# Optimization experiments

Hardware: AMD Instinct MI355X
Metric: run time of the kernel (lower is better)

## Reference

```python
import jax, jax.numpy as jnp
import numpy as np

B, T, V, D, U = 256, 1024, 6, 64, 64  # batch, seq, vocab, embed dim, lstm units


def _lstm_dir(x_seq, mask_seq, Wk, Wr, b, reverse):
    # x_seq: [B,T,D], mask_seq: [B,T] bool. Keras gate order: i, f, g(cell), o.
    Bc, Tc, _ = x_seq.shape
    Uc = Wr.shape[0]
    if reverse:
        x_seq = x_seq[:, ::-1, :]
        mask_seq = mask_seq[:, ::-1]
    # precompute input projections for all timesteps (one big GEMM)
    xproj = jnp.einsum('btd,dg->tbg', x_seq, Wk) + b          # [T,B,4U]
    m = jnp.swapaxes(mask_seq, 0, 1)[..., None]               # [T,B,1]

    def step(carry, inp):
        h, c = carry
        xp, mt = inp
        z = xp + h @ Wr                                        # [B,4U]
        i, f, g, o = jnp.split(z, 4, axis=-1)
        i = jax.nn.sigmoid(i)
        f = jax.nn.sigmoid(f)
        g = jnp.tanh(g)
        o = jax.nn.sigmoid(o)
        c_new = f * c + i * g
        h_new = o * jnp.tanh(c_new)
        # masked steps carry state through and repeat previous output
        h = jnp.where(mt, h_new, h)
        c = jnp.where(mt, c_new, c)
        return (h, c), h

    h0 = jnp.zeros((Bc, Uc), x_seq.dtype)
    _, ys = jax.lax.scan(step, (h0, h0), (xproj, m))           # ys: [T,B,U]
    ys = jnp.swapaxes(ys, 0, 1)                                # [B,T,U]
    if reverse:
        ys = ys[:, ::-1, :]
    return ys


def reference(tokens, emb, Wk_f, Wr_f, b_f, Wk_b, Wr_b, b_b, Wd, bd):
    x = emb[tokens]                                            # [B,T,D]
    mask = jnp.any(x != 0, axis=-1)                            # Masking(0): all-zero feature vec -> masked
    y_f = _lstm_dir(x, mask, Wk_f, Wr_f, b_f, reverse=False)   # [B,T,U]
    y_b = _lstm_dir(x, mask, Wk_b, Wr_b, b_b, reverse=True)    # [B,T,U]
    y = jnp.concatenate([y_f, y_b], axis=-1)                   # [B,T,2U]
    last = y[:, -1, :]                                         # [B,2U]
    return last @ Wd + bd                                      # [B,1]


def setup_inputs() -> dict:
    key = jax.random.key(0)
    ks = jax.random.split(key, 8)
    return {
        'tokens': jax.random.randint(ks[0], (B, T), 0, V, dtype=jnp.int32),
        'emb': jax.random.normal(ks[1], (V, D), dtype=jnp.float32),
        'Wk_f': jax.random.normal(ks[2], (D, 4 * U), dtype=jnp.float32) * 0.05,
        'Wr_f': jax.random.normal(ks[3], (U, 4 * U), dtype=jnp.float32) * 0.05,
        'b_f': jnp.zeros((4 * U,), dtype=jnp.float32),
        'Wk_b': jax.random.normal(ks[4], (D, 4 * U), dtype=jnp.float32) * 0.05,
        'Wr_b': jax.random.normal(ks[5], (U, 4 * U), dtype=jnp.float32) * 0.05,
        'b_b': jnp.zeros((4 * U,), dtype=jnp.float32),
        'Wd': jax.random.normal(ks[6], (2 * U, 1), dtype=jnp.float32) * 0.05,
        'bd': jnp.zeros((1,), dtype=jnp.float32),
    }
```

## Files before the change

### kernel.cpp

```cpp
#include <hip/hip_runtime.h>


constexpr int kB = 256;
constexpr int kT = 1024;
constexpr int kV = 6;
constexpr int kD = 64;
constexpr int kU = 64;
constexpr int kG = 256;

#define LOG2E 1.44269504f

typedef _Float16 v2h __attribute__((ext_vector_type(2)));

template <int CTRL>
__device__ __forceinline__ float dppf(float x) {
    return __int_as_float(
        __builtin_amdgcn_mov_dpp(__float_as_int(x), CTRL, 0xF, 0xF, true));
}
constexpr int kXor1 = 0xB1;
constexpr int kXor2 = 0x4E;
constexpr int kBc0 = 0x00, kBc1 = 0x55, kBc2 = 0xAA, kBc3 = 0xFF;

__device__ __forceinline__ float fast_rcp(float x) { return __builtin_amdgcn_rcpf(x); }
__device__ __forceinline__ float exp2_f(float x)   { return __builtin_amdgcn_exp2f(x); }
__device__ __forceinline__ float sig_f(float z)  { return fast_rcp(1.0f + exp2_f(-LOG2E * z)); }
__device__ __forceinline__ float tanh_f(float z) { return 2.0f * fast_rcp(1.0f + exp2_f(-2.0f * LOG2E * z)) - 1.0f; }

__device__ __forceinline__ v2h as_v2h(float x) { return __builtin_bit_cast(v2h, x); }

__global__ __launch_bounds__(256, 1) void bilstm_last_kernel(
    const int*   __restrict__ tokens,
    const float* __restrict__ emb,
    const float* __restrict__ Wk_f,
    const float* __restrict__ Wr_f,
    const float* __restrict__ b_f,
    const float* __restrict__ Wk_b,
    const float* __restrict__ b_b,
    const float* __restrict__ Wd,
    const float* __restrict__ bd,
    float*       __restrict__ out)
{
    __shared__ float s_emb[kV * kD];
    __shared__ float s_projP[kV * kG];
    __shared__ int   s_tok[kT];
    __shared__ _Float16 __align__(16) s_hh[2][kU];
    __shared__ float s_act[kG];

    const int b   = blockIdx.x;
    const int tid = threadIdx.x;
    const int l   = tid & 63;
    const int wv  = tid >> 6;
    const int s   = l & 3;
    const int k   = l >> 2;
    const int u   = wv * 16 + k;

    for (int i = tid; i < kV * kD; i += 256) s_emb[i] = emb[i];
    ((int4*)s_tok)[tid] = ((const int4*)(tokens + b * kT))[tid];
    if (tid < kU) { s_hh[0][tid] = (_Float16)0.f; s_hh[1][tid] = (_Float16)0.f; }
    __syncthreads();

    unsigned int mbv = 0;
#pragma unroll
    for (int v = 0; v < kV; ++v) {
        const unsigned long long bb = __ballot(s_emb[v * kD + l] != 0.0f);
        mbv |= (bb != 0ull) ? (1u << v) : 0u;
    }
    const unsigned int smb = __builtin_amdgcn_readfirstlane(mbv);

    const int tokL = s_tok[kT - 1];

    float a0 = b_f[tid], a1 = a0, a2 = a0, a3 = a0, a4 = a0, a5 = a0;
    float accb = b_b[tid];
    for (int d = 0; d < kD; ++d) {
        const float wkf = Wk_f[d * kG + tid];
        const float wkb = Wk_b[d * kG + tid];
        a0 = fmaf(s_emb[0 * kD + d], wkf, a0);
        a1 = fmaf(s_emb[1 * kD + d], wkf, a1);
        a2 = fmaf(s_emb[2 * kD + d], wkf, a2);
        a3 = fmaf(s_emb[3 * kD + d], wkf, a3);
        a4 = fmaf(s_emb[4 * kD + d], wkf, a4);
        a5 = fmaf(s_emb[5 * kD + d], wkf, a5);
        accb = fmaf(s_emb[tokL * kD + d], wkb, accb);
    }
    {
        const int g0 = tid >> 6, u0 = tid & 63, w0 = u0 >> 4, k0 = u0 & 15;
        const int q = w0 * 64 + k0 * 4 + g0;
        s_projP[0 * kG + q] = a0;
        s_projP[1 * kG + q] = a1;
        s_projP[2 * kG + q] = a2;
        s_projP[3 * kG + q] = a3;
        s_projP[4 * kG + q] = a4;
        s_projP[5 * kG + q] = a5;
    }

    float ab;
    if (tid < 128)      ab = sig_f(accb);
    else if (tid < 192) ab = tanh_f(accb);
    else                ab = sig_f(accb);
    s_act[tid] = ab;
    __syncthreads();
    float hb_val = 0.0f;
    if (tid < kU) {
        const float cb = s_act[tid] * s_act[2 * kU + tid];
        const float hb = s_act[3 * kU + tid] * tanh_f(cb);
        hb_val = ((smb >> tokL) & 1) ? hb : 0.0f;
    }

#define DECLH(g, p)                                                         \
    v2h wh##g##_##p;                                                        \
    wh##g##_##p.x = (_Float16)Wr_f[(16 * s + 2 * p + 0) * kG + (g * 64 + u)]; \
    wh##g##_##p.y = (_Float16)Wr_f[(16 * s + 2 * p + 1) * kG + (g * 64 + u)];
    DECLH(0,0) DECLH(0,1) DECLH(0,2) DECLH(0,3) DECLH(0,4) DECLH(0,5) DECLH(0,6) DECLH(0,7)
    DECLH(1,0) DECLH(1,1) DECLH(1,2) DECLH(1,3) DECLH(1,4) DECLH(1,5) DECLH(1,6) DECLH(1,7)
    DECLH(2,0) DECLH(2,1) DECLH(2,2) DECLH(2,3) DECLH(2,4) DECLH(2,5) DECLH(2,6) DECLH(2,7)
    DECLH(3,0) DECLH(3,1) DECLH(3,2) DECLH(3,3) DECLH(3,4) DECLH(3,5) DECLH(3,6) DECLH(3,7)
#undef DECLH

    const bool  isg    = (s == 2);
    const float aScale = isg ? -2.0f * LOG2E : -LOG2E;
    const float aMul   = isg ? 2.0f : 1.0f;
    const float aAdd   = isg ? -1.0f : 0.0f;

    float c = 0.0f, hreg = 0.0f;
    __syncthreads();

    int stok0 = __builtin_amdgcn_readfirstlane(s_tok[0]);
    float zcur = s_projP[stok0 * kG + tid];
    int   mskc = (smb >> stok0) & 1;
    int   stokA = __builtin_amdgcn_readfirstlane(s_tok[1]);

#define DOTG(g)                                                               \
        float pa##g = __builtin_amdgcn_fdot2(H0, wh##g##_0, 0.0f, false);     \
        float pb##g = __builtin_amdgcn_fdot2(H1, wh##g##_1, 0.0f, false);     \
        pa##g = __builtin_amdgcn_fdot2(H2, wh##g##_2, pa##g, false);          \
        pb##g = __builtin_amdgcn_fdot2(H3, wh##g##_3, pb##g, false);          \
        pa##g = __builtin_amdgcn_fdot2(H4, wh##g##_4, pa##g, false);          \
        pb##g = __builtin_amdgcn_fdot2(H5, wh##g##_5, pb##g, false);          \
        pa##g = __builtin_amdgcn_fdot2(H6, wh##g##_6, pa##g, false);          \
        pb##g = __builtin_amdgcn_fdot2(H7, wh##g##_7, pb##g, false);          \
        float p##g = pa##g + pb##g;

#define STEP(RP, WP, TT)                                                      \
    {                                                                         \
                        \
        const float4* hp = (const float4*)s_hh[RP];                           \
        const float4 hv0 = hp[s * 2 + 0];                                     \
        const float4 hv1 = hp[s * 2 + 1];                                     \
                    \
        const int   vtokB = s_tok[((TT) + 2) & (kT - 1)];                     \
        const float znext = s_projP[stokA * kG + tid];                        \
        const int   mskn  = (int)((smb >> stokA) & 1);                        \
        const v2h H0 = as_v2h(hv0.x), H1 = as_v2h(hv0.y);                     \
        const v2h H2 = as_v2h(hv0.z), H3 = as_v2h(hv0.w);                     \
        const v2h H4 = as_v2h(hv1.x), H5 = as_v2h(hv1.y);                     \
        const v2h H6 = as_v2h(hv1.z), H7 = as_v2h(hv1.w);                     \
        DOTG(0) DOTG(1) DOTG(2) DOTG(3)                                       \
                         \
        p0 += dppf<kXor1>(p0); p1 += dppf<kXor1>(p1);                         \
        p2 += dppf<kXor1>(p2); p3 += dppf<kXor1>(p3);                         \
        \
        float X = (s & 1) ? p1 : p0;                                          \
        float Y = (s & 1) ? p3 : p2;                                          \
        X += dppf<kXor2>(X); Y += dppf<kXor2>(Y);                             \
        const float z = ((s & 2) ? Y : X) + zcur;                             \
                                      \
        const float e = exp2_f(z * aScale);                                   \
        const float r = fast_rcp(1.0f + e);                                   \
        const float a = fmaf(r, aMul, aAdd);                                  \
                     \
        const float ai = dppf<kBc0>(a);                                       \
        const float af = dppf<kBc1>(a);                                       \
        const float ag = dppf<kBc2>(a);                                       \
        const float ao = dppf<kBc3>(a);                                       \
        const float cn = fmaf(af, c, ai * ag);                                \
        const float hn = ao * tanh_f(cn);                                     \
        if (mskc) { c = cn; hreg = hn; }                  \
        if (s == 0) s_hh[WP][u] = (_Float16)hreg;                             \
        __syncthreads();                                                      \
        zcur = znext; mskc = mskn;                                            \
        stokA = __builtin_amdgcn_readfirstlane(vtokB);                        \
    }

    for (int t = 0; t < kT; t += 2) {
        STEP(0, 1, t)
        STEP(1, 0, t + 1)
    }
#undef STEP
#undef DOTG

    if (s == 0) s_act[u] = hreg;
    __syncthreads();
    if (tid < kU) {
        float v = s_act[tid] * Wd[tid] + hb_val * Wd[kU + tid];
#pragma unroll
        for (int off = 32; off > 0; off >>= 1) v += __shfl_down(v, off, 64);
        if (tid == 0) out[b] = v + bd[0];
    }
}

extern "C" void kernel_launch(void* const* d_in, const int* in_sizes, int n_in,
                              void* d_out, int out_size, void* d_ws, size_t ws_size,
                              hipStream_t stream) {
    const int*   tokens = (const int*)d_in[0];
    const float* emb    = (const float*)d_in[1];
    const float* Wk_f   = (const float*)d_in[2];
    const float* Wr_f   = (const float*)d_in[3];
    const float* b_f    = (const float*)d_in[4];
    const float* Wk_b   = (const float*)d_in[5];
    const float* b_b    = (const float*)d_in[7];
    const float* Wd     = (const float*)d_in[8];
    const float* bd     = (const float*)d_in[9];
    float* out = (float*)d_out;

    bilstm_last_kernel<<<kB, 256, 0, stream>>>(
        tokens, emb, Wk_f, Wr_f, b_f, Wk_b, b_b, Wd, bd, out);
}
```

Measured before the change: 345.9 us.

## Run each batch row's recurrence in one wavefront without block barriers

```diff
diff --git a/kernel.cpp b/kernel.cpp
--- a/kernel.cpp
+++ b/kernel.cpp
@@ -12,15 +12,6 @@
 
 typedef _Float16 v2h __attribute__((ext_vector_type(2)));
 
-template <int CTRL>
-__device__ __forceinline__ float dppf(float x) {
-    return __int_as_float(
-        __builtin_amdgcn_mov_dpp(__float_as_int(x), CTRL, 0xF, 0xF, true));
-}
-constexpr int kXor1 = 0xB1;
-constexpr int kXor2 = 0x4E;
-constexpr int kBc0 = 0x00, kBc1 = 0x55, kBc2 = 0xAA, kBc3 = 0xFF;
-
 __device__ __forceinline__ float fast_rcp(float x) { return __builtin_amdgcn_rcpf(x); }
 __device__ __forceinline__ float exp2_f(float x)   { return __builtin_amdgcn_exp2f(x); }
 __device__ __forceinline__ float sig_f(float z)  { return fast_rcp(1.0f + exp2_f(-LOG2E * z)); }
@@ -28,7 +19,7 @@
 
 __device__ __forceinline__ v2h as_v2h(float x) { return __builtin_bit_cast(v2h, x); }
 
-__global__ __launch_bounds__(256, 1) void bilstm_last_kernel(
+__global__ __launch_bounds__(64, 1) void bilstm_last_kernel(
     const int*   __restrict__ tokens,
     const float* __restrict__ emb,
     const float* __restrict__ Wk_f,
@@ -41,23 +32,23 @@
     float*       __restrict__ out)
 {
     __shared__ float s_emb[kV * kD];
-    __shared__ float s_projP[kV * kG];
-    __shared__ int   s_tok[kT];
+    __shared__ float s_projPP[kV * kU * 4];
+    __shared__ int   __align__(16) s_tok[kT];
     __shared__ _Float16 __align__(16) s_hh[2][kU];
-    __shared__ float s_act[kG];
-
-    const int b   = blockIdx.x;
-    const int tid = threadIdx.x;
-    const int l   = tid & 63;
-    const int wv  = tid >> 6;
-    const int s   = l & 3;
-    const int k   = l >> 2;
-    const int u   = wv * 16 + k;
-
-    for (int i = tid; i < kV * kD; i += 256) s_emb[i] = emb[i];
-    ((int4*)s_tok)[tid] = ((const int4*)(tokens + b * kT))[tid];
-    if (tid < kU) { s_hh[0][tid] = (_Float16)0.f; s_hh[1][tid] = (_Float16)0.f; }
-    __syncthreads();
+
+    const int b = blockIdx.x;
+    const int l = threadIdx.x;
+
+#pragma unroll
+    for (int i = 0; i < kV * kD; i += 64) s_emb[i + l] = emb[i + l];
+    {
+        const int4* src = (const int4*)(tokens + b * kT);
+        int4* dst = (int4*)s_tok;
+#pragma unroll
+        for (int i = 0; i < 4; ++i) dst[64 * i + l] = src[64 * i + l];
+    }
+    s_hh[0][l] = (_Float16)0.f;
+    s_hh[1][l] = (_Float16)0.f;
 
     unsigned int mbv = 0;
 #pragma unroll
@@ -67,116 +58,113 @@
     }
     const unsigned int smb = __builtin_amdgcn_readfirstlane(mbv);
 
-    const int tokL = s_tok[kT - 1];
-
-    float a0 = b_f[tid], a1 = a0, a2 = a0, a3 = a0, a4 = a0, a5 = a0;
-    float accb = b_b[tid];
+    const int tokL = __builtin_amdgcn_readfirstlane(s_tok[kT - 1]);
+
+    float af[kV][4];
+    float ab4[4];
+#pragma unroll
+    for (int g = 0; g < 4; ++g) {
+        const float bf = b_f[g * kU + l];
+#pragma unroll
+        for (int v = 0; v < kV; ++v) af[v][g] = bf;
+        ab4[g] = b_b[g * kU + l];
+    }
+#pragma unroll 4
     for (int d = 0; d < kD; ++d) {
-        const float wkf = Wk_f[d * kG + tid];
-        const float wkb = Wk_b[d * kG + tid];
-        a0 = fmaf(s_emb[0 * kD + d], wkf, a0);
-        a1 = fmaf(s_emb[1 * kD + d], wkf, a1);
-        a2 = fmaf(s_emb[2 * kD + d], wkf, a2);
-        a3 = fmaf(s_emb[3 * kD + d], wkf, a3);
-        a4 = fmaf(s_emb[4 * kD + d], wkf, a4);
-        a5 = fmaf(s_emb[5 * kD + d], wkf, a5);
-        accb = fmaf(s_emb[tokL * kD + d], wkb, accb);
-    }
+        const float e0 = s_emb[0 * kD + d], e1 = s_emb[1 * kD + d];
+        const float e2 = s_emb[2 * kD + d], e3 = s_emb[3 * kD + d];
+        const float e4 = s_emb[4 * kD + d], e5 = s_emb[5 * kD + d];
+        const float eb = s_emb[tokL * kD + d];
+#pragma unroll
+        for (int g = 0; g < 4; ++g) {
+            const float wkf = Wk_f[d * kG + g * kU + l];
+            const float wkb = Wk_b[d * kG + g * kU + l];
+            af[0][g] = fmaf(e0, wkf, af[0][g]);
+            af[1][g] = fmaf(e1, wkf, af[1][g]);
+            af[2][g] = fmaf(e2, wkf, af[2][g]);
+            af[3][g] = fmaf(e3, wkf, af[3][g]);
+            af[4][g] = fmaf(e4, wkf, af[4][g]);
+            af[5][g] = fmaf(e5, wkf, af[5][g]);
+            ab4[g]   = fmaf(eb, wkb, ab4[g]);
+        }
+    }
+#pragma unroll
+    for (int v = 0; v < kV; ++v) {
+        float4 t4;
+        t4.x = af[v][0]; t4.y = af[v][1]; t4.z = af[v][2]; t4.w = af[v][3];
+        ((float4*)s_projPP)[v * kU + l] = t4;
+    }
+
+    float hb_val;
     {
-        const int g0 = tid >> 6, u0 = tid & 63, w0 = u0 >> 4, k0 = u0 & 15;
-        const int q = w0 * 64 + k0 * 4 + g0;
-        s_projP[0 * kG + q] = a0;
-        s_projP[1 * kG + q] = a1;
-        s_projP[2 * kG + q] = a2;
-        s_projP[3 * kG + q] = a3;
-        s_projP[4 * kG + q] = a4;
-        s_projP[5 * kG + q] = a5;
-    }
-
-    float ab;
-    if (tid < 128)      ab = sig_f(accb);
-    else if (tid < 192) ab = tanh_f(accb);
-    else                ab = sig_f(accb);
-    s_act[tid] = ab;
-    __syncthreads();
-    float hb_val = 0.0f;
-    if (tid < kU) {
-        const float cb = s_act[tid] * s_act[2 * kU + tid];
-        const float hb = s_act[3 * kU + tid] * tanh_f(cb);
+        const float ib = sig_f(ab4[0]);
+        const float gb = tanh_f(ab4[2]);
+        const float ob = sig_f(ab4[3]);
+        const float cb = ib * gb;
+        const float hb = ob * tanh_f(cb);
         hb_val = ((smb >> tokL) & 1) ? hb : 0.0f;
     }
 
-#define DECLH(g, p)                                                         \
-    v2h wh##g##_##p;                                                        \
-    wh##g##_##p.x = (_Float16)Wr_f[(16 * s + 2 * p + 0) * kG + (g * 64 + u)]; \
-    wh##g##_##p.y = (_Float16)Wr_f[(16 * s + 2 * p + 1) * kG + (g * 64 + u)];
-    DECLH(0,0) DECLH(0,1) DECLH(0,2) DECLH(0,3) DECLH(0,4) DECLH(0,5) DECLH(0,6) DECLH(0,7)
-    DECLH(1,0) DECLH(1,1) DECLH(1,2) DECLH(1,3) DECLH(1,4) DECLH(1,5) DECLH(1,6) DECLH(1,7)
-    DECLH(2,0) DECLH(2,1) DECLH(2,2) DECLH(2,3) DECLH(2,4) DECLH(2,5) DECLH(2,6) DECLH(2,7)
-    DECLH(3,0) DECLH(3,1) DECLH(3,2) DECLH(3,3) DECLH(3,4) DECLH(3,5) DECLH(3,6) DECLH(3,7)
-#undef DECLH
-
-    const bool  isg    = (s == 2);
-    const float aScale = isg ? -2.0f * LOG2E : -LOG2E;
-    const float aMul   = isg ? 2.0f : 1.0f;
-    const float aAdd   = isg ? -1.0f : 0.0f;
+    v2h wh[4][32];
+#pragma unroll
+    for (int g = 0; g < 4; ++g)
+#pragma unroll
+        for (int p = 0; p < 32; ++p) {
+            wh[g][p].x = (_Float16)Wr_f[(2 * p + 0) * kG + g * kU + l];
+            wh[g][p].y = (_Float16)Wr_f[(2 * p + 1) * kG + g * kU + l];
+        }
 
     float c = 0.0f, hreg = 0.0f;
-    __syncthreads();
 
     int stok0 = __builtin_amdgcn_readfirstlane(s_tok[0]);
-    float zcur = s_projP[stok0 * kG + tid];
-    int   mskc = (smb >> stok0) & 1;
-    int   stokA = __builtin_amdgcn_readfirstlane(s_tok[1]);
-
-#define DOTG(g)                                                               \
-        float pa##g = __builtin_amdgcn_fdot2(H0, wh##g##_0, 0.0f, false);     \
-        float pb##g = __builtin_amdgcn_fdot2(H1, wh##g##_1, 0.0f, false);     \
-        pa##g = __builtin_amdgcn_fdot2(H2, wh##g##_2, pa##g, false);          \
-        pb##g = __builtin_amdgcn_fdot2(H3, wh##g##_3, pb##g, false);          \
-        pa##g = __builtin_amdgcn_fdot2(H4, wh##g##_4, pa##g, false);          \
-        pb##g = __builtin_amdgcn_fdot2(H5, wh##g##_5, pb##g, false);          \
-        pa##g = __builtin_amdgcn_fdot2(H6, wh##g##_6, pa##g, false);          \
-        pb##g = __builtin_amdgcn_fdot2(H7, wh##g##_7, pb##g, false);          \
-        float p##g = pa##g + pb##g;
+    float4 zcur = ((const float4*)s_projPP)[stok0 * kU + l];
+    int mskc = (smb >> stok0) & 1;
+    int stokA = __builtin_amdgcn_readfirstlane(s_tok[1]);
+
+#define DOTG(g, seed, zout)                                                   \
+    {                                                                         \
+        float pa = __builtin_amdgcn_fdot2(H[0], wh[g][0], (seed), false);     \
+        float pb = __builtin_amdgcn_fdot2(H[1], wh[g][1], 0.0f, false);       \
+        _Pragma("unroll")                                                     \
+        for (int j = 1; j < 16; ++j) {                                        \
+            pa = __builtin_amdgcn_fdot2(H[2*j],   wh[g][2*j],   pa, false);   \
+            pb = __builtin_amdgcn_fdot2(H[2*j+1], wh[g][2*j+1], pb, false);   \
+        }                                                                     \
+        zout = pa + pb;                                                       \
+    }
 
 #define STEP(RP, WP, TT)                                                      \
     {                                                                         \
-                        \
+              \
         const float4* hp = (const float4*)s_hh[RP];                           \
-        const float4 hv0 = hp[s * 2 + 0];                                     \
-        const float4 hv1 = hp[s * 2 + 1];                                     \
-                    \
+        const float4 hv0 = hp[0], hv1 = hp[1], hv2 = hp[2], hv3 = hp[3];      \
+        const float4 hv4 = hp[4], hv5 = hp[5], hv6 = hp[6], hv7 = hp[7];      \
+                          \
         const int   vtokB = s_tok[((TT) + 2) & (kT - 1)];                     \
-        const float znext = s_projP[stokA * kG + tid];                        \
-        const int   mskn  = (int)((smb >> stokA) & 1);                        \
-        const v2h H0 = as_v2h(hv0.x), H1 = as_v2h(hv0.y);                     \
-        const v2h H2 = as_v2h(hv0.z), H3 = as_v2h(hv0.w);                     \
-        const v2h H4 = as_v2h(hv1.x), H5 = as_v2h(hv1.y);                     \
-        const v2h H6 = as_v2h(hv1.z), H7 = as_v2h(hv1.w);                     \
-        DOTG(0) DOTG(1) DOTG(2) DOTG(3)                                       \
-                         \
-        p0 += dppf<kXor1>(p0); p1 += dppf<kXor1>(p1);                         \
-        p2 += dppf<kXor1>(p2); p3 += dppf<kXor1>(p3);                         \
-        \
-        float X = (s & 1) ? p1 : p0;                                          \
-        float Y = (s & 1) ? p3 : p2;                                          \
-        X += dppf<kXor2>(X); Y += dppf<kXor2>(Y);                             \
-        const float z = ((s & 2) ? Y : X) + zcur;                             \
-                                      \
-        const float e = exp2_f(z * aScale);                                   \
-        const float r = fast_rcp(1.0f + e);                                   \
-        const float a = fmaf(r, aMul, aAdd);                                  \
-                     \
-        const float ai = dppf<kBc0>(a);                                       \
-        const float af = dppf<kBc1>(a);                                       \
-        const float ag = dppf<kBc2>(a);                                       \
-        const float ao = dppf<kBc3>(a);                                       \
-        const float cn = fmaf(af, c, ai * ag);                                \
+        const float4 znext = ((const float4*)s_projPP)[stokA * kU + l];       \
+        const int   mskn = (int)((smb >> stokA) & 1);                         \
+        v2h H[32];                                                            \
+        H[0]=as_v2h(hv0.x);  H[1]=as_v2h(hv0.y);  H[2]=as_v2h(hv0.z);  H[3]=as_v2h(hv0.w);  \
+        H[4]=as_v2h(hv1.x);  H[5]=as_v2h(hv1.y);  H[6]=as_v2h(hv1.z);  H[7]=as_v2h(hv1.w);  \
+        H[8]=as_v2h(hv2.x);  H[9]=as_v2h(hv2.y);  H[10]=as_v2h(hv2.z); H[11]=as_v2h(hv2.w); \
+        H[12]=as_v2h(hv3.x); H[13]=as_v2h(hv3.y); H[14]=as_v2h(hv3.z); H[15]=as_v2h(hv3.w); \
+        H[16]=as_v2h(hv4.x); H[17]=as_v2h(hv4.y); H[18]=as_v2h(hv4.z); H[19]=as_v2h(hv4.w); \
+        H[20]=as_v2h(hv5.x); H[21]=as_v2h(hv5.y); H[22]=as_v2h(hv5.z); H[23]=as_v2h(hv5.w); \
+        H[24]=as_v2h(hv6.x); H[25]=as_v2h(hv6.y); H[26]=as_v2h(hv6.z); H[27]=as_v2h(hv6.w); \
+        H[28]=as_v2h(hv7.x); H[29]=as_v2h(hv7.y); H[30]=as_v2h(hv7.z); H[31]=as_v2h(hv7.w); \
+        float zi, zf, zg, zo;                                                 \
+        DOTG(0, zcur.x, zi)                                                   \
+        DOTG(1, zcur.y, zf)                                                   \
+        DOTG(2, zcur.z, zg)                                                   \
+        DOTG(3, zcur.w, zo)                                                   \
+        const float ai  = sig_f(zi);                                          \
+        const float afv = sig_f(zf);                                          \
+        const float ag  = tanh_f(zg);                                         \
+        const float ao  = sig_f(zo);                                          \
+        const float cn = fmaf(afv, c, ai * ag);                               \
         const float hn = ao * tanh_f(cn);                                     \
         if (mskc) { c = cn; hreg = hn; }                  \
-        if (s == 0) s_hh[WP][u] = (_Float16)hreg;                             \
-        __syncthreads();                                                      \
+        s_hh[WP][l] = (_Float16)hreg;                                         \
         zcur = znext; mskc = mskn;                                            \
         stokA = __builtin_amdgcn_readfirstlane(vtokB);                        \
     }
@@ -188,14 +176,10 @@
 #undef STEP
 #undef DOTG
 
-    if (s == 0) s_act[u] = hreg;
-    __syncthreads();
-    if (tid < kU) {
-        float v = s_act[tid] * Wd[tid] + hb_val * Wd[kU + tid];
-#pragma unroll
-        for (int off = 32; off > 0; off >>= 1) v += __shfl_down(v, off, 64);
-        if (tid == 0) out[b] = v + bd[0];
-    }
+    float v = hreg * Wd[l] + hb_val * Wd[kU + l];
+#pragma unroll
+    for (int off = 32; off > 0; off >>= 1) v += __shfl_down(v, off, 64);
+    if (l == 0) out[b] = v + bd[0];
 }
 
 extern "C" void kernel_launch(void* const* d_in, const int* in_sizes, int n_in,
@@ -212,6 +196,6 @@
     const float* bd     = (const float*)d_in[9];
     float* out = (float*)d_out;
 
-    bilstm_last_kernel<<<kB, 256, 0, stream>>>(
+    bilstm_last_kernel<<<kB, 64, 0, stream>>>(
         tokens, emb, Wk_f, Wr_f, b_f, Wk_b, b_b, Wd, bd, out);
 }
```

Result: slower. 507.7 us (+46.8%).

## Keep per-token input projections in registers instead of LDS lookup table

Applied to the files above, without the earlier changes.

```diff
diff --git a/kernel.cpp b/kernel.cpp
--- a/kernel.cpp
+++ b/kernel.cpp
@@ -23,12 +23,13 @@
 
 __device__ __forceinline__ float fast_rcp(float x) { return __builtin_amdgcn_rcpf(x); }
 __device__ __forceinline__ float exp2_f(float x)   { return __builtin_amdgcn_exp2f(x); }
-__device__ __forceinline__ float sig_f(float z)  { return fast_rcp(1.0f + exp2_f(-LOG2E * z)); }
 __device__ __forceinline__ float tanh_f(float z) { return 2.0f * fast_rcp(1.0f + exp2_f(-2.0f * LOG2E * z)) - 1.0f; }
 
 __device__ __forceinline__ v2h as_v2h(float x) { return __builtin_bit_cast(v2h, x); }
 
-__global__ __launch_bounds__(256, 1) void bilstm_last_kernel(
+__global__ __launch_bounds__(256)
+__attribute__((amdgpu_waves_per_eu(1, 1)))
+void bilstm_last_kernel(
     const int*   __restrict__ tokens,
     const float* __restrict__ emb,
     const float* __restrict__ Wk_f,
@@ -41,10 +42,9 @@
     float*       __restrict__ out)
 {
     __shared__ float s_emb[kV * kD];
-    __shared__ float s_projP[kV * kG];
-    __shared__ int   s_tok[kT];
+    __shared__ int   __align__(16) s_tok[kT];
     __shared__ _Float16 __align__(16) s_hh[2][kU];
-    __shared__ float s_act[kG];
+    __shared__ float s_red[4];
 
     const int b   = blockIdx.x;
     const int tid = threadIdx.x;
@@ -53,10 +53,11 @@
     const int s   = l & 3;
     const int k   = l >> 2;
     const int u   = wv * 16 + k;
+    const int col = s * kU + u;
 
     for (int i = tid; i < kV * kD; i += 256) s_emb[i] = emb[i];
     ((int4*)s_tok)[tid] = ((const int4*)(tokens + b * kT))[tid];
-    if (tid < kU) { s_hh[0][tid] = (_Float16)0.f; s_hh[1][tid] = (_Float16)0.f; }
+    if (tid < 2 * kU) ((_Float16*)s_hh)[tid] = (_Float16)0.f;
     __syncthreads();
 
     unsigned int mbv = 0;
@@ -67,67 +68,69 @@
     }
     const unsigned int smb = __builtin_amdgcn_readfirstlane(mbv);
 
-    const int tokL = s_tok[kT - 1];
-
-    float a0 = b_f[tid], a1 = a0, a2 = a0, a3 = a0, a4 = a0, a5 = a0;
-    float accb = b_b[tid];
-    for (int d = 0; d < kD; ++d) {
-        const float wkf = Wk_f[d * kG + tid];
-        const float wkb = Wk_b[d * kG + tid];
-        a0 = fmaf(s_emb[0 * kD + d], wkf, a0);
-        a1 = fmaf(s_emb[1 * kD + d], wkf, a1);
-        a2 = fmaf(s_emb[2 * kD + d], wkf, a2);
-        a3 = fmaf(s_emb[3 * kD + d], wkf, a3);
-        a4 = fmaf(s_emb[4 * kD + d], wkf, a4);
-        a5 = fmaf(s_emb[5 * kD + d], wkf, a5);
-        accb = fmaf(s_emb[tokL * kD + d], wkb, accb);
-    }
+    const int tokL = __builtin_amdgcn_readfirstlane(s_tok[kT - 1]);
+
+    const bool  isg    = (s == 2);
+    const float aScale = isg ? -2.0f * LOG2E : -LOG2E;
+    const float aMul   = isg ? 2.0f : 1.0f;
+    const float aAdd   = isg ? -1.0f : 0.0f;
+
+    float pf0, pf1, pf2, pf3, pf4, pf5;
+    float ab;
     {
-        const int g0 = tid >> 6, u0 = tid & 63, w0 = u0 >> 4, k0 = u0 & 15;
-        const int q = w0 * 64 + k0 * 4 + g0;
-        s_projP[0 * kG + q] = a0;
-        s_projP[1 * kG + q] = a1;
-        s_projP[2 * kG + q] = a2;
-        s_projP[3 * kG + q] = a3;
-        s_projP[4 * kG + q] = a4;
-        s_projP[5 * kG + q] = a5;
-    }
-
-    float ab;
-    if (tid < 128)      ab = sig_f(accb);
-    else if (tid < 192) ab = tanh_f(accb);
-    else                ab = sig_f(accb);
-    s_act[tid] = ab;
-    __syncthreads();
-    float hb_val = 0.0f;
-    if (tid < kU) {
-        const float cb = s_act[tid] * s_act[2 * kU + tid];
-        const float hb = s_act[3 * kU + tid] * tanh_f(cb);
+        float afv[kV];
+        const float bf = b_f[col];
+#pragma unroll
+        for (int v = 0; v < kV; ++v) afv[v] = bf;
+        ab = b_b[col];
+#pragma unroll 4
+        for (int d = 0; d < kD; ++d) {
+            const float wkf = Wk_f[d * kG + col];
+            const float wkb = Wk_b[d * kG + col];
+            afv[0] = fmaf(s_emb[0 * kD + d], wkf, afv[0]);
+            afv[1] = fmaf(s_emb[1 * kD + d], wkf, afv[1]);
+            afv[2] = fmaf(s_emb[2 * kD + d], wkf, afv[2]);
+            afv[3] = fmaf(s_emb[3 * kD + d], wkf, afv[3]);
+            afv[4] = fmaf(s_emb[4 * kD + d], wkf, afv[4]);
+            afv[5] = fmaf(s_emb[5 * kD + d], wkf, afv[5]);
+            ab     = fmaf(s_emb[tokL * kD + d], wkb, ab);
+        }
+        pf0 = afv[0]; pf1 = afv[1]; pf2 = afv[2];
+        pf3 = afv[3]; pf4 = afv[4]; pf5 = afv[5];
+    }
+    auto sel6 = [&](int t) -> float {
+        return t == 0 ? pf0 : t == 1 ? pf1 : t == 2 ? pf2
+             : t == 3 ? pf3 : t == 4 ? pf4 : pf5;
+    };
+
+    float hb_val;
+    {
+        const float e = exp2_f(ab * aScale);
+        const float r = fast_rcp(1.0f + e);
+        const float a = fmaf(r, aMul, aAdd);
+        const float cb = dppf<kBc0>(a) * dppf<kBc2>(a);
+        const float hb = dppf<kBc3>(a) * tanh_f(cb);
         hb_val = ((smb >> tokL) & 1) ? hb : 0.0f;
     }
 
-#define DECLH(g, p)                                                         \
-    v2h wh##g##_##p;                                                        \
-    wh##g##_##p.x = (_Float16)Wr_f[(16 * s + 2 * p + 0) * kG + (g * 64 + u)]; \
-    wh##g##_##p.y = (_Float16)Wr_f[(16 * s + 2 * p + 1) * kG + (g * 64 + u)];
+#define DECLH(g, p)                                                           \
+    v2h wh##g##_##p;                                                          \
+    wh##g##_##p.x = (_Float16)Wr_f[(16 * s + 2 * (p) + 0) * kG + ((g) * 64 + u)]; \
+    wh##g##_##p.y = (_Float16)Wr_f[(16 * s + 2 * (p) + 1) * kG + ((g) * 64 + u)];
     DECLH(0,0) DECLH(0,1) DECLH(0,2) DECLH(0,3) DECLH(0,4) DECLH(0,5) DECLH(0,6) DECLH(0,7)
     DECLH(1,0) DECLH(1,1) DECLH(1,2) DECLH(1,3) DECLH(1,4) DECLH(1,5) DECLH(1,6) DECLH(1,7)
     DECLH(2,0) DECLH(2,1) DECLH(2,2) DECLH(2,3) DECLH(2,4) DECLH(2,5) DECLH(2,6) DECLH(2,7)
     DECLH(3,0) DECLH(3,1) DECLH(3,2) DECLH(3,3) DECLH(3,4) DECLH(3,5) DECLH(3,6) DECLH(3,7)
 #undef DECLH
 
-    const bool  isg    = (s == 2);
-    const float aScale = isg ? -2.0f * LOG2E : -LOG2E;
-    const float aMul   = isg ? 2.0f : 1.0f;
-    const float aAdd   = isg ? -1.0f : 0.0f;
-
     float c = 0.0f, hreg = 0.0f;
-    __syncthreads();
-
-    int stok0 = __builtin_amdgcn_readfirstlane(s_tok[0]);
-    float zcur = s_projP[stok0 * kG + tid];
-    int   mskc = (smb >> stok0) & 1;
-    int   stokA = __builtin_amdgcn_readfirstlane(s_tok[1]);
+
+    int st0 = __builtin_amdgcn_readfirstlane(s_tok[0]);
+    int st1 = __builtin_amdgcn_readfirstlane(s_tok[1]);
+    int st2 = __builtin_amdgcn_readfirstlane(s_tok[2]);
+    int st3 = __builtin_amdgcn_readfirstlane(s_tok[3]);
+    float zc0 = sel6(st0), zc1 = sel6(st1);
+    int   mk0 = (smb >> st0) & 1, mk1 = (smb >> st1) & 1;
 
 #define DOTG(g)                                                               \
         float pa##g = __builtin_amdgcn_fdot2(H0, wh##g##_0, 0.0f, false);     \
@@ -140,29 +143,24 @@
         pb##g = __builtin_amdgcn_fdot2(H7, wh##g##_7, pb##g, false);          \
         float p##g = pa##g + pb##g;
 
-#define STEP(RP, WP, TT)                                                      \
+#define STEP(RP, WP, ZC, MK)                                                  \
     {                                                                         \
-                        \
+           \
         const float4* hp = (const float4*)s_hh[RP];                           \
         const float4 hv0 = hp[s * 2 + 0];                                     \
         const float4 hv1 = hp[s * 2 + 1];                                     \
-                    \
-        const int   vtokB = s_tok[((TT) + 2) & (kT - 1)];                     \
-        const float znext = s_projP[stokA * kG + tid];                        \
-        const int   mskn  = (int)((smb >> stokA) & 1);                        \
         const v2h H0 = as_v2h(hv0.x), H1 = as_v2h(hv0.y);                     \
         const v2h H2 = as_v2h(hv0.z), H3 = as_v2h(hv0.w);                     \
         const v2h H4 = as_v2h(hv1.x), H5 = as_v2h(hv1.y);                     \
         const v2h H6 = as_v2h(hv1.z), H7 = as_v2h(hv1.w);                     \
         DOTG(0) DOTG(1) DOTG(2) DOTG(3)                                       \
-                         \
+            \
         p0 += dppf<kXor1>(p0); p1 += dppf<kXor1>(p1);                         \
         p2 += dppf<kXor1>(p2); p3 += dppf<kXor1>(p3);                         \
-        \
         float X = (s & 1) ? p1 : p0;                                          \
         float Y = (s & 1) ? p3 : p2;                                          \
         X += dppf<kXor2>(X); Y += dppf<kXor2>(Y);                             \
-        const float z = ((s & 2) ? Y : X) + zcur;                             \
+        const float z = ((s & 2) ? Y : X) + (ZC);                             \
                                       \
         const float e = exp2_f(z * aScale);                                   \
         const float r = fast_rcp(1.0f + e);                                   \
@@ -174,28 +172,33 @@
         const float ao = dppf<kBc3>(a);                                       \
         const float cn = fmaf(af, c, ai * ag);                                \
         const float hn = ao * tanh_f(cn);                                     \
-        if (mskc) { c = cn; hreg = hn; }                  \
+        if (MK) { c = cn; hreg = hn; }                    \
         if (s == 0) s_hh[WP][u] = (_Float16)hreg;                             \
         __syncthreads();                                                      \
-        zcur = znext; mskc = mskn;                                            \
-        stokA = __builtin_amdgcn_readfirstlane(vtokB);                        \
-    }
-
+    }
+
+#pragma unroll 1
     for (int t = 0; t < kT; t += 2) {
-        STEP(0, 1, t)
-        STEP(1, 0, t + 1)
+        STEP(0, 1, zc0, mk0)
+        const int2 vt = *((const int2*)(s_tok + ((t + 4) & (kT - 1))));
+        const float zn0 = sel6(st2); const int mn0 = (smb >> st2) & 1;
+        const float zn1 = sel6(st3); const int mn1 = (smb >> st3) & 1;
+        STEP(1, 0, zc1, mk1)
+        st2 = __builtin_amdgcn_readfirstlane(vt.x);
+        st3 = __builtin_amdgcn_readfirstlane(vt.y);
+        zc0 = zn0; zc1 = zn1; mk0 = mn0; mk1 = mn1;
     }
 #undef STEP
 #undef DOTG
 
-    if (s == 0) s_act[u] = hreg;
-    __syncthreads();
-    if (tid < kU) {
-        float v = s_act[tid] * Wd[tid] + hb_val * Wd[kU + tid];
+    {
+        float v = (s == 0) ? (hreg * Wd[u] + hb_val * Wd[kU + u]) : 0.0f;
 #pragma unroll
         for (int off = 32; off > 0; off >>= 1) v += __shfl_down(v, off, 64);
-        if (tid == 0) out[b] = v + bd[0];
-    }
+        if (l == 0) s_red[wv] = v;
+    }
+    __syncthreads();
+    if (tid == 0) out[b] = (s_red[0] + s_red[1]) + (s_red[2] + s_red[3]) + bd[0];
 }
 
 extern "C" void kernel_launch(void* const* d_in, const int* in_sizes, int n_in,
```

Measured after the change: 402.7 us. 16.4% more time.
